# Kernel optimization log

Measured on AMD Instinct MI355X. Metric: run time of the kernel, lower is better.

## Reference

```python
import jax, jax.numpy as jnp
import numpy as np

NUM_NODES, FEAT_DIM, DIM, CLIPS = 100000, 128, 128, 8
S1, S2 = 10, 10
B, L = 1024, 8


def setup_inputs() -> dict:
    key = jax.random.key(0)
    k1, k2, k3, k4, k5 = jax.random.split(key, 5)
    features = jax.random.normal(k1, (NUM_NODES, FEAT_DIM), dtype=jnp.float32)
    # xavier-uniform-ish init for the per-clip projection
    local_weight = jax.random.normal(k2, (CLIPS, DIM, FEAT_DIM), dtype=jnp.float32) * (2.0 / (DIM + FEAT_DIM)) ** 0.5
    nodes = jax.random.randint(k3, (B, L), 0, NUM_NODES, dtype=jnp.int64 if jax.config.jax_enable_x64 else jnp.int32)
    neigh1 = jax.random.randint(k4, (NUM_NODES, S1), 0, NUM_NODES, dtype=nodes.dtype)
    neigh2 = jax.random.randint(k5, (NUM_NODES, S2), 0, NUM_NODES, dtype=nodes.dtype)
    return {"features": features, "local_weight": local_weight, "nodes": nodes,
            "neigh1": neigh1, "neigh2": neigh2}


def reference(features, local_weight, nodes, neigh1, neigh2):
    b, l = nodes.shape
    nf = nodes.reshape(-1)                     # [N] flat nodes
    # hop-0: raw features
    feat_self = features[nf]                   # [N, d]
    # hop-1: mean over sampled 1-hop neighbors (agg1)
    feats1 = features[neigh1[nf]].mean(axis=1)  # [N, s1, d] -> [N, d]
    # hop-2: mean over sampled 2-hop neighbors of agg1 outputs (agg2)
    two_hop = neigh1[neigh2[nf]]               # [N, s2, s1]
    feats2 = features[two_hop].mean(axis=2).mean(axis=1)  # [N, d]
    # per-clip projection: einsum('ckd,dn->ckn').permute(2,0,1) == 'ckd,nd->nck'
    outs = [jnp.einsum('ckd,nd->nck', local_weight, f)
            for f in (feats1, feats2, feat_self)]         # each [N, clips, dim]
    local = jnp.concatenate(outs, axis=-1)                # [N, clips, 3*dim]
    local = local.reshape(b, l, local_weight.shape[0], -1)
    return jax.nn.relu(local)
```

## Files before the change

kernel.cpp:

```cpp
#include <hip/hip_runtime.h>

typedef __attribute__((ext_vector_type(8))) short bf16x8;
typedef __attribute__((ext_vector_type(4))) float f32x4;

static constexpr int N_NODES = 8192;
static constexpr int FEAT    = 128;
static constexpr int NB      = 16;
static constexpr int NBLK    = N_NODES / NB;
static constexpr int XS      = 136;
static constexpr int F8_BLOCKS = 3125;

__device__ __forceinline__ unsigned short f2bf(float f) {
    unsigned u = __builtin_bit_cast(unsigned, f);
    u += 0x7FFFu + ((u >> 16) & 1u);
    return (unsigned short)(u >> 16);
}
__device__ __forceinline__ unsigned f2fp8(float f) {
    unsigned u = __builtin_bit_cast(unsigned, f);
    unsigned s = (u >> 24) & 0x80u;
    float af = __builtin_bit_cast(float, u & 0x7fffffffu);
    if (!(af < 448.f)) af = 448.f;
    unsigned q = __builtin_bit_cast(unsigned, af * 0x1p-120f);
    unsigned b = (q + 0x7FFFFu + ((q >> 20) & 1u)) >> 20;
    return s | b;
}
__device__ __forceinline__ void acc8f8(float* a, const uint2 v) {
#pragma unroll
    for (int i = 0; i < 4; ++i) {
        unsigned t = v.x << (24 - 8 * i);
        unsigned w = (unsigned)((int)t >> 4) & 0x87F00000u;
        a[i] = fmaf(__builtin_bit_cast(float, w), 0x1p120f, a[i]);
    }
#pragma unroll
    for (int i = 0; i < 4; ++i) {
        unsigned t = v.y << (24 - 8 * i);
        unsigned w = (unsigned)((int)t >> 4) & 0x87F00000u;
        a[4 + i] = fmaf(__builtin_bit_cast(float, w), 0x1p120f, a[4 + i]);
    }
}
__device__ __forceinline__ uint4 pack8(const float* a, float sc) {
    uint4 o;
    o.x = (unsigned)f2bf(a[0] * sc) | ((unsigned)f2bf(a[1] * sc) << 16);
    o.y = (unsigned)f2bf(a[2] * sc) | ((unsigned)f2bf(a[3] * sc) << 16);
    o.z = (unsigned)f2bf(a[4] * sc) | ((unsigned)f2bf(a[5] * sc) << 16);
    o.w = (unsigned)f2bf(a[6] * sc) | ((unsigned)f2bf(a[7] * sc) << 16);
    return o;
}

__global__ void __launch_bounds__(256) pack_all(
    const float* __restrict__ feat, const float* __restrict__ lw,
    unsigned char* __restrict__ T8, unsigned short* __restrict__ Wp)
{
    const int b = blockIdx.x;
    if (b < F8_BLOCKS) {
        const size_t i = (size_t)b * 256 + threadIdx.x;
        const f32x4* src = (const f32x4*)feat + i * 4;
        uint4 p;
        unsigned* pw = (unsigned*)&p;
#pragma unroll
        for (int h = 0; h < 4; ++h) {
            const f32x4 v = __builtin_nontemporal_load(src + h);
            pw[h] = f2fp8(v[0]) | (f2fp8(v[1]) << 8) | (f2fp8(v[2]) << 16) | (f2fp8(v[3]) << 24);
        }
        ((uint4*)T8)[i] = p;
    } else {
        const int i = (b - F8_BLOCKS) * 256 + threadIdx.x;
        const float4 v = ((const float4*)lw)[i];
        ushort4 o;
        o.x = f2bf(v.x); o.y = f2bf(v.y); o.z = f2bf(v.z); o.w = f2bf(v.w);
        ((ushort4*)Wp)[i] = o;
    }
}

__global__ void __launch_bounds__(256) fused_enc(
    const unsigned char*  __restrict__ T8,
    const float* __restrict__ featF,
    const int*   __restrict__ nodes,
    const int*   __restrict__ n1,
    const int*   __restrict__ n2,
    const unsigned short* __restrict__ Wp,
    float* __restrict__ out)
{
    __shared__ int nfs[NB];
    __shared__ int sm_m[NB][10];
    __shared__ int idx[NB][112];
    __shared__ unsigned short X[3 * NB][XS];

    const int blk = blockIdx.x;
    const int tid = threadIdx.x;

    if (tid < NB) nfs[tid] = nodes[blk * NB + tid];
    __syncthreads();
    if (tid < NB * 10) {
        const int i = tid / 10, s = tid - (tid / 10) * 10;
        idx[i][s] = n1[nfs[i] * 10 + s];
    }
    if (tid >= 96) {
        const int t = tid - 96;
        const int i = t / 10, s = t - (t / 10) * 10;
        sm_m[i][s] = n2[nfs[i] * 10 + s];
    }
    if (tid < NB) idx[tid][110] = nfs[tid];
    __syncthreads();
    for (int t = tid; t < NB * 100; t += 256) {
        const int i = t / 100, rr = t - (t / 100) * 100;
        idx[i][10 + rr] = n1[sm_m[i][rr / 10] * 10 + (rr - (rr / 10) * 10)];
    }
    __syncthreads();

    {
        const int g = tid >> 4;
        const int l = tid & 15;
        const unsigned char* Tl8 = T8 + l * 8;

        float aA[8] = {0,0,0,0,0,0,0,0};
        float aB[8] = {0,0,0,0,0,0,0,0};

        {
            uint2 v[10];
#pragma unroll
            for (int s = 0; s < 10; ++s)
                v[s] = *(const uint2*)(Tl8 + (size_t)idx[g][s] * FEAT);
#pragma unroll
            for (int s = 0; s < 10; ++s) acc8f8(aA, v[s]);
        }
#pragma unroll
        for (int c = 1; c <= 10; ++c) {
            uint2 v[10];
#pragma unroll
            for (int s = 0; s < 10; ++s)
                v[s] = *(const uint2*)(Tl8 + (size_t)idx[g][c * 10 + s] * FEAT);
#pragma unroll
            for (int s = 0; s < 10; ++s) acc8f8(aB, v[s]);
        }
        *(uint4*)&X[g * 3 + 0][l * 8] = pack8(aA, 0.1f);
        *(uint4*)&X[g * 3 + 1][l * 8] = pack8(aB, 0.01f);

        const float* Fs = featF + (size_t)idx[g][110] * FEAT + l * 8;
        const f32x4 s0 = *(const f32x4*)Fs;
        const f32x4 s1 = *(const f32x4*)(Fs + 4);
        float aS[8] = {s0[0], s0[1], s0[2], s0[3], s1[0], s1[1], s1[2], s1[3]};
        *(uint4*)&X[g * 3 + 2][l * 8] = pack8(aS, 1.0f);
    }
    __syncthreads();

    const int wave = tid >> 6;
    const int lane = tid & 63;
    const int r = lane & 15;
    const int q = lane >> 4;

#pragma unroll
    for (int ch = 0; ch < 4; ++ch) {
        const int yBase = wave * 256 + ch * 64;
        f32x4 acc[3][4];
#pragma unroll
        for (int mt = 0; mt < 3; ++mt)
#pragma unroll
            for (int nj = 0; nj < 4; ++nj) acc[mt][nj] = (f32x4){0.f, 0.f, 0.f, 0.f};

#pragma unroll
        for (int k0 = 0; k0 < 4; ++k0) {
            bf16x8 a[3], b[4];
#pragma unroll
            for (int mt = 0; mt < 3; ++mt)
                a[mt] = *(const bf16x8*)&X[mt * 16 + r][k0 * 32 + q * 8];
#pragma unroll
            for (int nj = 0; nj < 4; ++nj)
                b[nj] = *(const bf16x8*)(Wp + (size_t)(yBase + nj * 16 + r) * FEAT
                                            + q * 8 + k0 * 32);
#pragma unroll
            for (int mt = 0; mt < 3; ++mt)
#pragma unroll
                for (int nj = 0; nj < 4; ++nj)
                    acc[mt][nj] = __builtin_amdgcn_mfma_f32_16x16x32_bf16(
                        a[mt], b[nj], acc[mt][nj], 0, 0, 0);
        }

#pragma unroll
        for (int mt = 0; mt < 3; ++mt) {
#pragma unroll
            for (int i = 0; i < 4; ++i) {
                const int xl = mt * 16 + q * 4 + i;
                const int nl = xl / 3;
                const int j  = xl - nl * 3;
                float* orow = out + (size_t)(blk * NB + nl) * 3072 + j * 128;
#pragma unroll
                for (int nj = 0; nj < 4; ++nj) {
                    const int y = yBase + nj * 16 + r;
                    const int c = y >> 7;
                    const int k = y & 127;
                    orow[c * 384 + k] = fmaxf(acc[mt][nj][i], 0.f);
                }
            }
        }
    }
}

extern "C" void kernel_launch(void* const* d_in, const int* in_sizes, int n_in,
                              void* d_out, int out_size, void* d_ws, size_t ws_size,
                              hipStream_t stream) {
    const float* features = (const float*)d_in[0];
    const float* lw       = (const float*)d_in[1];
    const int*   nodes    = (const int*)d_in[2];
    const int*   n1       = (const int*)d_in[3];
    const int*   n2       = (const int*)d_in[4];
    float*       out      = (float*)d_out;

    unsigned short* Wp = (unsigned short*)d_ws;
    unsigned char*  T8 = (unsigned char*)(Wp + (size_t)1024 * FEAT);

    pack_all<<<F8_BLOCKS + 128, 256, 0, stream>>>(features, lw, T8, Wp);
    fused_enc<<<NBLK, 256, 0, stream>>>(T8, features, nodes, n1, n2, Wp, out);
}
```

Measured before the change: 66.11 us.

## Halve nodes per block and split two-hop gather across thread pairs

Result: slower. 82.30 us (+24.5%).

```diff
diff --git a/kernel.cpp b/kernel.cpp
--- a/kernel.cpp
+++ b/kernel.cpp
@@ -5,7 +5,7 @@
 
 static constexpr int N_NODES = 8192;
 static constexpr int FEAT    = 128;
-static constexpr int NB      = 16;
+static constexpr int NB      = 8;
 static constexpr int NBLK    = N_NODES / NB;
 static constexpr int XS      = 136;
 static constexpr int F8_BLOCKS = 3125;
@@ -84,23 +84,24 @@
     __shared__ int nfs[NB];
     __shared__ int sm_m[NB][10];
     __shared__ int idx[NB][112];
-    __shared__ unsigned short X[3 * NB][XS];
+    __shared__ unsigned short X[32][XS];
+    __shared__ float red[NB][FEAT];
 
     const int blk = blockIdx.x;
     const int tid = threadIdx.x;
 
     if (tid < NB) nfs[tid] = nodes[blk * NB + tid];
     __syncthreads();
-    if (tid < NB * 10) {
+    if (tid < 80) {
         const int i = tid / 10, s = tid - (tid / 10) * 10;
         idx[i][s] = n1[nfs[i] * 10 + s];
-    }
-    if (tid >= 96) {
-        const int t = tid - 96;
+    } else if (tid < 160) {
+        const int t = tid - 80;
         const int i = t / 10, s = t - (t / 10) * 10;
         sm_m[i][s] = n2[nfs[i] * 10 + s];
-    }
-    if (tid < NB) idx[tid][110] = nfs[tid];
+    } else if (tid < 160 + NB) {
+        idx[tid - 160][110] = nfs[tid - 160];
+    }
     __syncthreads();
     for (int t = tid; t < NB * 100; t += 256) {
         const int i = t / 100, rr = t - (t / 100) * 100;
@@ -109,38 +110,59 @@
     __syncthreads();
 
     {
-        const int g = tid >> 4;
-        const int l = tid & 15;
+        const int grp  = tid >> 4;
+        const int node = grp >> 1;
+        const int half = grp & 1;
+        const int l    = tid & 15;
         const unsigned char* Tl8 = T8 + l * 8;
 
         float aA[8] = {0,0,0,0,0,0,0,0};
         float aB[8] = {0,0,0,0,0,0,0,0};
 
-        {
-            uint2 v[10];
-#pragma unroll
-            for (int s = 0; s < 10; ++s)
-                v[s] = *(const uint2*)(Tl8 + (size_t)idx[g][s] * FEAT);
-#pragma unroll
-            for (int s = 0; s < 10; ++s) acc8f8(aA, v[s]);
-        }
-#pragma unroll
-        for (int c = 1; c <= 10; ++c) {
-            uint2 v[10];
-#pragma unroll
-            for (int s = 0; s < 10; ++s)
-                v[s] = *(const uint2*)(Tl8 + (size_t)idx[g][c * 10 + s] * FEAT);
-#pragma unroll
-            for (int s = 0; s < 10; ++s) acc8f8(aB, v[s]);
-        }
-        *(uint4*)&X[g * 3 + 0][l * 8] = pack8(aA, 0.1f);
-        *(uint4*)&X[g * 3 + 1][l * 8] = pack8(aB, 0.01f);
-
-        const float* Fs = featF + (size_t)idx[g][110] * FEAT + l * 8;
-        const f32x4 s0 = *(const f32x4*)Fs;
-        const f32x4 s1 = *(const f32x4*)(Fs + 4);
-        float aS[8] = {s0[0], s0[1], s0[2], s0[3], s1[0], s1[1], s1[2], s1[3]};
-        *(uint4*)&X[g * 3 + 2][l * 8] = pack8(aS, 1.0f);
+        if (!half) {
+            {
+                uint2 v[10];
+#pragma unroll
+                for (int s = 0; s < 10; ++s)
+                    v[s] = *(const uint2*)(Tl8 + (size_t)idx[node][s] * FEAT);
+#pragma unroll
+                for (int s = 0; s < 10; ++s) acc8f8(aA, v[s]);
+            }
+#pragma unroll
+            for (int c = 1; c <= 5; ++c) {
+                uint2 v[10];
+#pragma unroll
+                for (int s = 0; s < 10; ++s)
+                    v[s] = *(const uint2*)(Tl8 + (size_t)idx[node][c * 10 + s] * FEAT);
+#pragma unroll
+                for (int s = 0; s < 10; ++s) acc8f8(aB, v[s]);
+            }
+        } else {
+#pragma unroll
+            for (int c = 6; c <= 10; ++c) {
+                uint2 v[10];
+#pragma unroll
+                for (int s = 0; s < 10; ++s)
+                    v[s] = *(const uint2*)(Tl8 + (size_t)idx[node][c * 10 + s] * FEAT);
+#pragma unroll
+                for (int s = 0; s < 10; ++s) acc8f8(aB, v[s]);
+            }
+#pragma unroll
+            for (int h = 0; h < 2; ++h)
+                *(f32x4*)&red[node][l * 8 + h * 4] = *(const f32x4*)&aB[h * 4];
+        }
+        __syncthreads();
+        if (!half) {
+#pragma unroll
+            for (int h = 0; h < 8; ++h) aB[h] += red[node][l * 8 + h];
+            *(uint4*)&X[node * 3 + 0][l * 8] = pack8(aA, 0.1f);
+            *(uint4*)&X[node * 3 + 1][l * 8] = pack8(aB, 0.01f);
+            const float* Fs = featF + (size_t)idx[node][110] * FEAT + l * 8;
+            const f32x4 s0 = *(const f32x4*)Fs;
+            const f32x4 s1 = *(const f32x4*)(Fs + 4);
+            float aS[8] = {s0[0], s0[1], s0[2], s0[3], s1[0], s1[1], s1[2], s1[3]};
+            *(uint4*)&X[node * 3 + 2][l * 8] = pack8(aS, 1.0f);
+        }
     }
     __syncthreads();
 
@@ -152,24 +174,24 @@
 #pragma unroll
     for (int ch = 0; ch < 4; ++ch) {
         const int yBase = wave * 256 + ch * 64;
-        f32x4 acc[3][4];
-#pragma unroll
-        for (int mt = 0; mt < 3; ++mt)
+        f32x4 acc[2][4];
+#pragma unroll
+        for (int mt = 0; mt < 2; ++mt)
 #pragma unroll
             for (int nj = 0; nj < 4; ++nj) acc[mt][nj] = (f32x4){0.f, 0.f, 0.f, 0.f};
 
 #pragma unroll
         for (int k0 = 0; k0 < 4; ++k0) {
-            bf16x8 a[3], b[4];
-#pragma unroll
-            for (int mt = 0; mt < 3; ++mt)
+            bf16x8 a[2], b[4];
+#pragma unroll
+            for (int mt = 0; mt < 2; ++mt)
                 a[mt] = *(const bf16x8*)&X[mt * 16 + r][k0 * 32 + q * 8];
 #pragma unroll
             for (int nj = 0; nj < 4; ++nj)
                 b[nj] = *(const bf16x8*)(Wp + (size_t)(yBase + nj * 16 + r) * FEAT
                                             + q * 8 + k0 * 32);
 #pragma unroll
-            for (int mt = 0; mt < 3; ++mt)
+            for (int mt = 0; mt < 2; ++mt)
 #pragma unroll
                 for (int nj = 0; nj < 4; ++nj)
                     acc[mt][nj] = __builtin_amdgcn_mfma_f32_16x16x32_bf16(
@@ -177,19 +199,21 @@
         }
 
 #pragma unroll
-        for (int mt = 0; mt < 3; ++mt) {
+        for (int mt = 0; mt < 2; ++mt) {
 #pragma unroll
             for (int i = 0; i < 4; ++i) {
                 const int xl = mt * 16 + q * 4 + i;
-                const int nl = xl / 3;
-                const int j  = xl - nl * 3;
-                float* orow = out + (size_t)(blk * NB + nl) * 3072 + j * 128;
-#pragma unroll
-                for (int nj = 0; nj < 4; ++nj) {
-                    const int y = yBase + nj * 16 + r;
-                    const int c = y >> 7;
-                    const int k = y & 127;
-                    orow[c * 384 + k] = fmaxf(acc[mt][nj][i], 0.f);
+                if (xl < 3 * NB) {
+                    const int nl = xl / 3;
+                    const int j  = xl - nl * 3;
+                    float* orow = out + (size_t)(blk * NB + nl) * 3072 + j * 128;
+#pragma unroll
+                    for (int nj = 0; nj < 4; ++nj) {
+                        const int y = yBase + nj * 16 + r;
+                        const int c = y >> 7;
+                        const int k = y & 127;
+                        orow[c * 384 + k] = fmaxf(acc[mt][nj][i], 0.f);
+                    }
                 }
             }
         }
```
